# Kernel tuning notes

Hardware: AMD Instinct MI355X
Metric: run time of the kernel (lower is better)

## Reference

```python
import jax, jax.numpy as jnp
import numpy as np

T, B, D, H = 512, 64, 1024, 8
DH = D // H
LN_EPS = 1e-5


def setup_inputs() -> dict:
    ks = jax.random.split(jax.random.key(0), 12)
    s = 1.0 / np.sqrt(D)
    return {
        "x_real": jax.random.normal(ks[0], (T, B, D), jnp.float32),
        "x_imag": jax.random.normal(ks[1], (T, B, D), jnp.float32),
        "value_state": jnp.zeros((B, H, DH), jnp.float32),
        "t": jnp.arange(T, dtype=jnp.int64) if jax.config.jax_enable_x64 else jnp.arange(T, dtype=jnp.int32),
        # ComplexLinear input_proj (bias=True): weight layout [out, in] like torch
        "Wr_in": jax.random.normal(ks[2], (D, D), jnp.float32) * s,
        "Wi_in": jax.random.normal(ks[3], (D, D), jnp.float32) * s,
        "br_in": jax.random.normal(ks[4], (D,), jnp.float32) * 0.01,
        "bi_in": jax.random.normal(ks[5], (D,), jnp.float32) * 0.01,
        # LayerNorm affine
        "ln_gamma": jnp.ones((D,), jnp.float32),
        "ln_beta": jnp.zeros((D,), jnp.float32),
        # QKV linear (bias=False), torch layout [3D, D]
        "W_qkv": jax.random.normal(ks[6], (3 * D, D), jnp.float32) * s,
        # per-head EMA gate logits: log(alpha/(1-alpha)) with alpha=0.9
        "log_alpha": jnp.full((H,), float(np.log(0.9 / 0.1)), jnp.float32),
        # ComplexLinear output_proj (bias=False)
        "Wr_out": jax.random.normal(ks[7], (D, D), jnp.float32) * s,
        "Wi_out": jax.random.normal(ks[8], (D, D), jnp.float32) * s,
    }


def reference(x_real, x_imag, value_state, t, Wr_in, Wi_in, br_in, bi_in,
              ln_gamma, ln_beta, W_qkv, log_alpha, Wr_out, Wi_out):
    scale = jnp.asarray(np.sqrt(DH), x_real.dtype)
    alpha = jax.nn.sigmoid(log_alpha)[None, :, None]  # [1,H,1]

    def step(state, xs):
        xr, xi = xs  # [B,D] each
        # ComplexLinear input projection
        pr = xr @ Wr_in.T - xi @ Wi_in.T + br_in
        pi = xr @ Wi_in.T + xi @ Wr_in.T + bi_in
        xc = pr + pi
        # LayerNorm over last dim
        mu = xc.mean(-1, keepdims=True)
        var = ((xc - mu) ** 2).mean(-1, keepdims=True)
        xc = (xc - mu) * jax.lax.rsqrt(var + LN_EPS) * ln_gamma + ln_beta
        # QKV
        qkv = (xc @ W_qkv.T).reshape(-1, 3, H, DH)
        q, k, v = qkv[:, 0], qkv[:, 1], qkv[:, 2]  # [B,H,DH]
        # per-head sigmoid-gated EMA state update
        new_state = alpha * v + (1.0 - alpha) * state
        gate = jax.nn.sigmoid(jnp.sum(q * k, axis=-1, keepdims=True) / scale)  # [B,H,1]
        retrieved = (gate * new_state).reshape(-1, D)
        # ComplexLinear output projection with zero imaginary input
        return new_state, (retrieved @ Wr_out.T, retrieved @ Wi_out.T)

    final_state, (out_real, out_imag) = jax.lax.scan(step, value_state, (x_real, x_imag))
    return out_real, out_imag, final_state
```

## Files before the change

### kernel.cpp

```cpp
#include <hip/hip_runtime.h>
#include <stdint.h>

#define T_DIM 512
#define B_DIM 64
#define D_DIM 1024
#define H_DIM 8
#define DH_DIM 128
#define MROWS (T_DIM * B_DIM)

typedef unsigned short u16;
typedef __attribute__((ext_vector_type(8))) __bf16 bf16x8;
typedef __attribute__((ext_vector_type(4))) float f32x4;
typedef __attribute__((ext_vector_type(16))) float f32x16;

__device__ __forceinline__ u16 f2bf(float f) {
  union { float f; uint32_t u; } v; v.f = f;
  uint32_t u = v.u;
  u += 0x7fffu + ((u >> 16) & 1u);
  return (u16)(u >> 16);
}
__device__ __forceinline__ float bf2f(u16 h) {
  union { uint32_t u; float f; } v; v.u = ((uint32_t)h) << 16;
  return v.f;
}

__device__ __forceinline__ void gload16(const void* g, void* l) {
  __builtin_amdgcn_global_load_lds(
      (const __attribute__((address_space(1))) uint32_t*)g,
      (__attribute__((address_space(3))) uint32_t*)l, 16, 0, 0);
}

#define SB()  __builtin_amdgcn_sched_barrier(0)
#define BAR() __builtin_amdgcn_s_barrier()
#define VM4() asm volatile("s_waitcnt vmcnt(4)" ::: "memory")
#define VM6() asm volatile("s_waitcnt vmcnt(6)" ::: "memory")
#define PRIO1() __builtin_amdgcn_s_setprio(1)
#define PRIO0() __builtin_amdgcn_s_setprio(0)


__global__ void cast_bf16_kernel(const float* __restrict__ in, u16* __restrict__ out, size_t n8) {
  size_t i = (size_t)blockIdx.x * blockDim.x + threadIdx.x;
  const size_t stride = (size_t)gridDim.x * blockDim.x;
  for (; i < n8; i += stride) {
    const float4 a = ((const float4*)in)[i * 2];
    const float4 b = ((const float4*)in)[i * 2 + 1];
    union { u16 h[8]; uint4 u; } o;
    o.h[0] = f2bf(a.x); o.h[1] = f2bf(a.y); o.h[2] = f2bf(a.z); o.h[3] = f2bf(a.w);
    o.h[4] = f2bf(b.x); o.h[5] = f2bf(b.y); o.h[6] = f2bf(b.z); o.h[7] = f2bf(b.w);
    ((uint4*)out)[i] = o.u;
  }
}

__global__ void prep_wc_kernel(const float* __restrict__ Wr, const float* __restrict__ Wi,
                               u16* __restrict__ Wc) {
  const int idx = blockIdx.x * 256 + threadIdx.x;
  const int n = idx >> 11;
  const int k = idx & 2047;
  const int kk = k & 1023;
  const float a = Wr[n * 1024 + kk], b = Wi[n * 1024 + kk];
  Wc[idx] = f2bf(k < 1024 ? a + b : a - b);
}

__global__ void prep_bc_kernel(const float* __restrict__ br, const float* __restrict__ bi,
                               float* __restrict__ bc) {
  const int i = blockIdx.x * 256 + threadIdx.x;
  if (i < D_DIM) bc[i] = br[i] + bi[i];
}


__device__ __forceinline__ void readF(bf16x8 (&d)[2][2], const u16* s, int rowoff, int la32, int puA) {
#pragma unroll
  for (int mf = 0; mf < 2; ++mf)
#pragma unroll
    for (int kk = 0; kk < 2; ++kk)
      d[mf][kk] = *(const bf16x8*)(s + (rowoff + mf * 32 + la32) * 32 + (puA ^ (kk << 4)));
}

__device__ __forceinline__ void mfma8(f32x16 (&acc)[4][2], const bf16x8 (&a)[2][2],
                                      const bf16x8 (&b)[2][2], int QM) {
#pragma unroll
  for (int kk = 0; kk < 2; ++kk)
#pragma unroll
    for (int mf = 0; mf < 2; ++mf)
#pragma unroll
      for (int nf = 0; nf < 2; ++nf)
        acc[QM * 2 + mf][nf] =
            __builtin_amdgcn_mfma_f32_32x32x16_bf16(a[mf][kk], b[nf][kk], acc[QM * 2 + mf][nf], 0, 0, 0);
}

template <int EPI>
__global__ __launch_bounds__(512, 2) void gemm256_kernel(
    const u16* __restrict__ A0, const u16* __restrict__ A1, int kSplit, int lda,
    const u16* __restrict__ Bw, int ldb,
    const float* __restrict__ bias,
    void* __restrict__ C0, void* __restrict__ C1, void* __restrict__ C2,
    int ldc, int K, int nColBlk)
{
  extern __shared__ u16 lds[];
  const int tid  = threadIdx.x;
  const int lane = tid & 63;
  const int w    = tid >> 6;
  const int wr   = w >> 2;
  const int wc   = w & 3;

  const int bid   = blockIdx.x;
  const int xcd   = bid & 7;
  const int local = bid >> 3;
  const int rowL  = local / nColBlk;
  const int colB  = local - rowL * nColBlk;
  const size_t rowBase = (size_t)(xcd * 16 + rowL) * 256;
  const size_t colBase = (size_t)colB * 256;

  f32x16 acc[4][2];
#pragma unroll
  for (int i = 0; i < 4; ++i)
#pragma unroll
    for (int j = 0; j < 2; ++j)
#pragma unroll
      for (int e = 0; e < 16; ++e) acc[i][j][e] = 0.f;

  const int NT = K >> 6;
  const int la32 = lane & 31;
  const int g2   = lane >> 5;
  const int f    = (la32 & 3) ^ ((la32 >> 2) & 3);
  const int puA  = ((g2 ^ f) << 3);

  auto stageA = [&](int buf, int ks, int t) {
    if (t >= NT) t = 0;
    const int kb = t * 64;
    const u16* Ab; int kc;
    if (kb < kSplit) { Ab = A0; kc = kb; } else { Ab = A1; kc = kb - kSplit; }
    u16* dst = lds + buf * 32768 + ks * 8192;
#pragma unroll
    for (int i2 = 0; i2 < 2; ++i2) {
      const int l = i2 * 512 + tid, r = l >> 2, p = l & 3;
      const int lu = p ^ (r & 3) ^ ((r >> 2) & 3);
      gload16(Ab + (rowBase + r) * (size_t)lda + kc + ks * 32 + lu * 8, dst + l * 8);
    }
  };
  auto stageB = [&](int buf, int ks, int t) {
    if (t >= NT) t = 0;
    const int kb = t * 64;
    u16* dst = lds + buf * 32768 + 16384 + ks * 8192;
#pragma unroll
    for (int i2 = 0; i2 < 2; ++i2) {
      const int l = i2 * 512 + tid, r = l >> 2, p = l & 3;
      const int lu = p ^ (r & 3) ^ ((r >> 2) & 3);
      gload16(Bw + (colBase + r) * (size_t)ldb + kb + ks * 32 + lu * 8, dst + l * 8);
    }
  };

  const u16* sA_b0k0 = lds;
  const u16* sA_b0k1 = lds + 8192;
  const u16* sB_b0k0 = lds + 16384;
  const u16* sB_b0k1 = lds + 16384 + 8192;
  const u16* sA_b1k0 = lds + 32768;
  const u16* sA_b1k1 = lds + 32768 + 8192;
  const u16* sB_b1k0 = lds + 32768 + 16384;
  const u16* sB_b1k1 = lds + 32768 + 16384 + 8192;
  const int rA0 = wr * 128;
  const int rA1 = wr * 128 + 64;
  const int rB  = wc * 64;

  stageA(0, 0, 0); stageB(0, 0, 0); stageA(0, 1, 0); stageB(0, 1, 0);
  stageA(1, 0, 1); stageB(1, 0, 1);
  VM4();
  SB(); BAR(); SB();

  bf16x8 a0[2][2], a1[2][2], bbE[2][2], bbO[2][2];
  const int NIT = NT >> 1;
  for (int i = 0; i < NIT; ++i) {
    const int u = 2 * i, v = 2 * i + 1;
    readF(a0,  sA_b0k0, rA0, la32, puA);
    readF(bbE, sB_b0k0, rB,  la32, puA);
    readF(a1,  sA_b0k0, rA1, la32, puA);
    stageA(1, 1, v);
    SB(); BAR(); SB();
    PRIO1(); mfma8(acc, a0, bbE, 0); PRIO0(); SB();
    BAR(); SB();
    readF(a0,  sA_b0k1, rA0, la32, puA);
    readF(bbO, sB_b0k1, rB,  la32, puA);
    stageB(1, 1, v);
    SB(); BAR(); SB();
    PRIO1(); mfma8(acc, a1, bbE, 1); PRIO0(); SB();
    BAR(); SB();
    readF(a1,  sA_b0k1, rA1, la32, puA);
    stageA(0, 0, u + 2);
    SB(); BAR(); SB();
    PRIO1(); mfma8(acc, a0, bbO, 0); PRIO0(); SB();
    VM6();
    BAR(); SB();
    readF(a0,  sA_b1k0, rA0, la32, puA);
    readF(bbE, sB_b1k0, rB,  la32, puA);
    stageB(0, 0, u + 2);
    SB(); BAR(); SB();
    PRIO1(); mfma8(acc, a1, bbO, 1); PRIO0(); SB();
    VM4();
    BAR(); SB();
    readF(a1,  sA_b1k0, rA1, la32, puA);
    stageA(0, 1, u + 2);
    SB(); BAR(); SB();
    PRIO1(); mfma8(acc, a0, bbE, 0); PRIO0(); SB();
    BAR(); SB();
    readF(a0,  sA_b1k1, rA0, la32, puA);
    readF(bbO, sB_b1k1, rB,  la32, puA);
    stageB(0, 1, u + 2);
    SB(); BAR(); SB();
    PRIO1(); mfma8(acc, a1, bbE, 1); PRIO0(); SB();
    BAR(); SB();
    readF(a1,  sA_b1k1, rA1, la32, puA);
    stageA(1, 0, v + 2);
    SB(); BAR(); SB();
    PRIO1(); mfma8(acc, a0, bbO, 0); PRIO0(); SB();
    BAR(); SB();
    stageB(1, 0, v + 2);
    SB(); BAR(); SB();
    PRIO1(); mfma8(acc, a1, bbO, 1); PRIO0(); SB();
    VM4();
    BAR(); SB();
  }

  const int seg = (int)(colBase >> 10);
  const size_t colSeg = colBase & 1023;
  void* Cout;
  if (EPI == 3)      Cout = (seg == 0) ? C0 : (seg == 1) ? C1 : C2;
  else if (EPI == 2) Cout = (seg == 0) ? C0 : C1;
  else               Cout = C0;

#pragma unroll
  for (int mi = 0; mi < 4; ++mi)
#pragma unroll
    for (int ni = 0; ni < 2; ++ni) {
      const int cn = wc * 64 + ni * 32 + la32;
      const float badd = (EPI == 1) ? bias[colBase + cn] : 0.0f;
      const size_t col = colSeg + cn;
#pragma unroll
      for (int r = 0; r < 16; ++r) {
        const size_t row = rowBase + wr * 128 + mi * 32 + (r & 3) + 8 * (r >> 2) + 4 * g2;
        const float v = acc[mi][ni][r] + badd;
        if (EPI == 2) ((float*)Cout)[row * (size_t)ldc + col] = v;
        else          ((u16*)Cout)[row * (size_t)ldc + col] = f2bf(v);
      }
    }
}


__global__ __launch_bounds__(256) void ln_kernel(u16* __restrict__ xc,
    const float* __restrict__ gamma, const float* __restrict__ beta)
{
  const size_t row = blockIdx.x;
  u16* p = xc + row * D_DIM;
  const int tid = threadIdx.x;
  const int c = tid * 4;
  const uint2 raw = *(const uint2*)(p + c);
  const float v0 = bf2f((u16)(raw.x & 0xffff)), v1 = bf2f((u16)(raw.x >> 16));
  const float v2 = bf2f((u16)(raw.y & 0xffff)), v3 = bf2f((u16)(raw.y >> 16));
  float s = v0 + v1 + v2 + v3;
  float q = v0 * v0 + v1 * v1 + v2 * v2 + v3 * v3;
#pragma unroll
  for (int o = 32; o > 0; o >>= 1) { s += __shfl_xor(s, o); q += __shfl_xor(q, o); }
  __shared__ float red[8];
  if ((tid & 63) == 0) { red[(tid >> 6) * 2] = s; red[(tid >> 6) * 2 + 1] = q; }
  __syncthreads();
  s = red[0] + red[2] + red[4] + red[6];
  q = red[1] + red[3] + red[5] + red[7];
  const float mu = s * (1.0f / D_DIM);
  const float var = q * (1.0f / D_DIM) - mu * mu;
  const float rstd = 1.0f / sqrtf(var + 1e-5f);
  const float y0 = (v0 - mu) * rstd * gamma[c] + beta[c];
  const float y1 = (v1 - mu) * rstd * gamma[c + 1] + beta[c + 1];
  const float y2 = (v2 - mu) * rstd * gamma[c + 2] + beta[c + 2];
  const float y3 = (v3 - mu) * rstd * gamma[c + 3] + beta[c + 3];
  const uint32_t o0 = (uint32_t)f2bf(y0) | ((uint32_t)f2bf(y1) << 16);
  const uint32_t o1 = (uint32_t)f2bf(y2) | ((uint32_t)f2bf(y3) << 16);
  *(uint2*)(p + c) = make_uint2(o0, o1);
}


__global__ __launch_bounds__(256) void gate_kernel(
    const u16* __restrict__ Q, const u16* __restrict__ Kb, float* __restrict__ gate)
{
  const int gw = blockIdx.x * 4 + (threadIdx.x >> 6);
  const int lane = threadIdx.x & 63;
  const size_t row = (size_t)(gw >> 3);
  const int h = gw & 7;
  const size_t off = row * D_DIM + h * DH_DIM + lane * 2;
  const uint32_t qr = *(const uint32_t*)(Q + off);
  const uint32_t kr = *(const uint32_t*)(Kb + off);
  float d = bf2f((u16)(qr & 0xffff)) * bf2f((u16)(kr & 0xffff))
          + bf2f((u16)(qr >> 16))    * bf2f((u16)(kr >> 16));
#pragma unroll
  for (int o = 32; o > 0; o >>= 1) d += __shfl_xor(d, o);
  if (lane == 0) {
    const float x = d * 0.08838834764831845f;
    gate[gw] = 1.0f / (1.0f + expf(-x));
  }
}


__global__ __launch_bounds__(256) void scan_kernel(
    const u16* __restrict__ vb, const float* __restrict__ gate,
    const float* __restrict__ vstate, const float* __restrict__ log_alpha,
    u16* __restrict__ ret, float* __restrict__ fstate)
{
  const int gid = blockIdx.x * 256 + threadIdx.x;
  const int b = gid >> 10;
  const int c = gid & 1023;
  const int h = c >> 7;
  const float alpha = 1.0f / (1.0f + expf(-log_alpha[h]));
  const float oma = 1.0f - alpha;
  float state = vstate[gid];
  const u16* vp = vb + (size_t)b * D_DIM + c;
  u16* rp = ret + (size_t)b * D_DIM + c;
  const float* gp = gate + b * H_DIM + h;
#pragma unroll 4
  for (int t = 0; t < T_DIM; ++t) {
    const float v = bf2f(vp[(size_t)t * (B_DIM * D_DIM)]);
    const float g = gp[(size_t)t * (B_DIM * H_DIM)];
    state = alpha * v + oma * state;
    rp[(size_t)t * (B_DIM * D_DIM)] = f2bf(g * state);
  }
  fstate[gid] = state;
}


extern "C" void kernel_launch(void* const* d_in, const int* in_sizes, int n_in,
                              void* d_out, int out_size, void* d_ws, size_t ws_size,
                              hipStream_t stream) {
  const float* x_real      = (const float*)d_in[0];
  const float* x_imag      = (const float*)d_in[1];
  const float* value_state = (const float*)d_in[2];
  const float* Wr_in  = (const float*)d_in[4];
  const float* Wi_in  = (const float*)d_in[5];
  const float* br_in  = (const float*)d_in[6];
  const float* bi_in  = (const float*)d_in[7];
  const float* ln_g   = (const float*)d_in[8];
  const float* ln_b   = (const float*)d_in[9];
  const float* W_qkv  = (const float*)d_in[10];
  const float* log_alpha = (const float*)d_in[11];
  const float* Wr_out = (const float*)d_in[12];
  const float* Wi_out = (const float*)d_in[13];

  float* out_real = (float*)d_out;
  float* out_imag = out_real + (size_t)MROWS * D_DIM;
  float* fstate   = out_imag + (size_t)MROWS * D_DIM;

  u16* R0a = (u16*)d_out;
  u16* xc  = (u16*)((char*)d_out + (size_t)MROWS * D_DIM * 2);
  u16* Vb  = (u16*)out_imag;

  char* ws = (char*)d_ws;
  size_t off = 0;
  auto alloc = [&](size_t bytes) { void* p = ws + off; off += (bytes + 255) & ~(size_t)255; return p; };
  u16*   Wc    = (u16*)alloc((size_t)1024 * 2048 * 2);
  u16*   Wqkvb = (u16*)alloc((size_t)3072 * 1024 * 2);
  u16*   Wob   = (u16*)alloc((size_t)2048 * 1024 * 2);
  float* bc    = (float*)alloc((size_t)D_DIM * 4);
  u16*   R0b   = (u16*)alloc((size_t)MROWS * D_DIM * 2);
  float* gate  = (float*)alloc((size_t)MROWS * H_DIM * 4);

  const int LDSB = 131072;
  hipFuncSetAttribute((const void*)gemm256_kernel<1>, hipFuncAttributeMaxDynamicSharedMemorySize, LDSB);
  hipFuncSetAttribute((const void*)gemm256_kernel<2>, hipFuncAttributeMaxDynamicSharedMemorySize, LDSB);
  hipFuncSetAttribute((const void*)gemm256_kernel<3>, hipFuncAttributeMaxDynamicSharedMemorySize, LDSB);

  prep_wc_kernel<<<(1024 * 2048) / 256, 256, 0, stream>>>(Wr_in, Wi_in, Wc);
  prep_bc_kernel<<<4, 256, 0, stream>>>(br_in, bi_in, bc);
  cast_bf16_kernel<<<1536, 256, 0, stream>>>(W_qkv, Wqkvb, (size_t)3072 * 1024 / 8);
  cast_bf16_kernel<<<512, 256, 0, stream>>>(Wr_out, Wob, (size_t)1024 * 1024 / 8);
  cast_bf16_kernel<<<512, 256, 0, stream>>>(Wi_out, Wob + (size_t)1024 * 1024, (size_t)1024 * 1024 / 8);
  cast_bf16_kernel<<<4096, 256, 0, stream>>>(x_real, R0a, (size_t)MROWS * D_DIM / 8);
  cast_bf16_kernel<<<4096, 256, 0, stream>>>(x_imag, R0b, (size_t)MROWS * D_DIM / 8);

  gemm256_kernel<1><<<dim3(128 * 4), 512, LDSB, stream>>>(
      R0a, R0b, 1024, 1024, Wc, 2048, bc, xc, nullptr, nullptr, 1024, 2048, 4);
  ln_kernel<<<MROWS, 256, 0, stream>>>(xc, ln_g, ln_b);
  gemm256_kernel<3><<<dim3(128 * 12), 512, LDSB, stream>>>(
      xc, xc, 1024, 1024, Wqkvb, 1024, nullptr, R0a, R0b, Vb, 1024, 1024, 12);
  gate_kernel<<<(MROWS * H_DIM) / 4, 256, 0, stream>>>(R0a, R0b, gate);
  scan_kernel<<<(B_DIM * D_DIM) / 256, 256, 0, stream>>>(Vb, gate, value_state, log_alpha, R0b, fstate);
  gemm256_kernel<2><<<dim3(128 * 8), 512, LDSB, stream>>>(
      R0b, R0b, 1024, 1024, Wob, 1024, nullptr, out_real, out_imag, nullptr, 1024, 1024, 8);
}
```

Measured before the change: 750.8 us.

## Split EMA scan into chunked two-pass scan and merge prep/cast launches

Replaces the sequential 512-step per-channel scan, which ran only 256 blocks, with a two-pass chunked scan. Pass one computes a local carry for each of 8 time chunks, and pass two combines the prior carries using oma^64 before rescanning its chunk, giving 8x more parallelism. The v tensor is read twice and a carry buffer is added. The separate weight-prep and cast kernels are also merged into two launches to cut launch overhead.

```diff
diff --git a/kernel.cpp b/kernel.cpp
--- a/kernel.cpp
+++ b/kernel.cpp
@@ -38,33 +38,49 @@
 #define PRIO0() __builtin_amdgcn_s_setprio(0)
 
 
-__global__ void cast_bf16_kernel(const float* __restrict__ in, u16* __restrict__ out, size_t n8) {
-  size_t i = (size_t)blockIdx.x * blockDim.x + threadIdx.x;
-  const size_t stride = (size_t)gridDim.x * blockDim.x;
-  for (; i < n8; i += stride) {
-    const float4 a = ((const float4*)in)[i * 2];
-    const float4 b = ((const float4*)in)[i * 2 + 1];
-    union { u16 h[8]; uint4 u; } o;
-    o.h[0] = f2bf(a.x); o.h[1] = f2bf(a.y); o.h[2] = f2bf(a.z); o.h[3] = f2bf(a.w);
-    o.h[4] = f2bf(b.x); o.h[5] = f2bf(b.y); o.h[6] = f2bf(b.z); o.h[7] = f2bf(b.w);
-    ((uint4*)out)[i] = o.u;
-  }
-}
-
-__global__ void prep_wc_kernel(const float* __restrict__ Wr, const float* __restrict__ Wi,
-                               u16* __restrict__ Wc) {
-  const int idx = blockIdx.x * 256 + threadIdx.x;
-  const int n = idx >> 11;
-  const int k = idx & 2047;
-  const int kk = k & 1023;
-  const float a = Wr[n * 1024 + kk], b = Wi[n * 1024 + kk];
-  Wc[idx] = f2bf(k < 1024 ? a + b : a - b);
-}
-
-__global__ void prep_bc_kernel(const float* __restrict__ br, const float* __restrict__ bi,
-                               float* __restrict__ bc) {
-  const int i = blockIdx.x * 256 + threadIdx.x;
-  if (i < D_DIM) bc[i] = br[i] + bi[i];
+__device__ __forceinline__ void cast8(const float* __restrict__ in, u16* __restrict__ out, size_t i) {
+  const float4 a = ((const float4*)in)[i * 2];
+  const float4 b = ((const float4*)in)[i * 2 + 1];
+  union { u16 h[8]; uint4 u; } o;
+  o.h[0] = f2bf(a.x); o.h[1] = f2bf(a.y); o.h[2] = f2bf(a.z); o.h[3] = f2bf(a.w);
+  o.h[4] = f2bf(b.x); o.h[5] = f2bf(b.y); o.h[6] = f2bf(b.z); o.h[7] = f2bf(b.w);
+  ((uint4*)out)[i] = o.u;
+}
+
+__global__ void prep_all_kernel(const float* __restrict__ Wr, const float* __restrict__ Wi,
+                                const float* __restrict__ br, const float* __restrict__ bi,
+                                const float* __restrict__ Wqkv,
+                                const float* __restrict__ Wro, const float* __restrict__ Wio,
+                                u16* __restrict__ Wc, float* __restrict__ bc,
+                                u16* __restrict__ Wqkvb, u16* __restrict__ Wob) {
+  const int blk = blockIdx.x;
+  if (blk < 8192) {
+    const int idx = blk * 256 + threadIdx.x;
+    const int n = idx >> 11;
+    const int k = idx & 2047;
+    const int kk = k & 1023;
+    const float a = Wr[n * 1024 + kk], b = Wi[n * 1024 + kk];
+    Wc[idx] = f2bf(k < 1024 ? a + b : a - b);
+  } else if (blk < 9728) {
+    cast8(Wqkv, Wqkvb, (size_t)(blk - 8192) * 256 + threadIdx.x);
+  } else if (blk < 10240) {
+    cast8(Wro, Wob, (size_t)(blk - 9728) * 256 + threadIdx.x);
+  } else if (blk < 10752) {
+    cast8(Wio, Wob + (size_t)1024 * 1024, (size_t)(blk - 10240) * 256 + threadIdx.x);
+  } else {
+    const int i = (blk - 10752) * 256 + threadIdx.x;
+    if (i < D_DIM) bc[i] = br[i] + bi[i];
+  }
+}
+
+__global__ void cast2_kernel(const float* __restrict__ xr, const float* __restrict__ xi,
+                             u16* __restrict__ outr, u16* __restrict__ outi) {
+  int blk = blockIdx.x;
+  const float* src; u16* dst;
+  if (blk < 4096) { src = xr; dst = outr; } else { src = xi; dst = outi; blk -= 4096; }
+  const size_t base = (size_t)blk * 1024 + threadIdx.x;
+#pragma unroll
+  for (int q = 0; q < 4; ++q) cast8(src, dst, base + q * 256);
 }
 
 
@@ -298,29 +314,65 @@
 }
 
 
-__global__ __launch_bounds__(256) void scan_kernel(
-    const u16* __restrict__ vb, const float* __restrict__ gate,
-    const float* __restrict__ vstate, const float* __restrict__ log_alpha,
-    u16* __restrict__ ret, float* __restrict__ fstate)
+__global__ __launch_bounds__(256) void scan1_kernel(
+    const u16* __restrict__ vb, const float* __restrict__ log_alpha,
+    float* __restrict__ carry)
 {
-  const int gid = blockIdx.x * 256 + threadIdx.x;
+  const int j  = blockIdx.x >> 7;
+  const int th = (blockIdx.x & 127) * 256 + threadIdx.x;
+  const int gid = th * 2;
   const int b = gid >> 10;
   const int c = gid & 1023;
   const int h = c >> 7;
   const float alpha = 1.0f / (1.0f + expf(-log_alpha[h]));
   const float oma = 1.0f - alpha;
-  float state = vstate[gid];
-  const u16* vp = vb + (size_t)b * D_DIM + c;
-  u16* rp = ret + (size_t)b * D_DIM + c;
-  const float* gp = gate + b * H_DIM + h;
+  const u16* vp = vb + ((size_t)(4096 * j + b)) * 1024 + c;
+  float s0 = 0.f, s1 = 0.f;
+#pragma unroll 8
+  for (int i = 0; i < 64; ++i) {
+    const uint32_t uv = *(const uint32_t*)(vp + (size_t)i * 65536);
+    s0 = alpha * bf2f((u16)(uv & 0xffff)) + oma * s0;
+    s1 = alpha * bf2f((u16)(uv >> 16))    + oma * s1;
+  }
+  *(float2*)(carry + (size_t)j * 65536 + gid) = make_float2(s0, s1);
+}
+
+__global__ __launch_bounds__(256) void scan2_kernel(
+    const u16* __restrict__ vb, const float* __restrict__ gate,
+    const float* __restrict__ vstate, const float* __restrict__ log_alpha,
+    const float* __restrict__ carry,
+    u16* __restrict__ ret, float* __restrict__ fstate)
+{
+  const int j  = blockIdx.x >> 7;
+  const int th = (blockIdx.x & 127) * 256 + threadIdx.x;
+  const int gid = th * 2;
+  const int b = gid >> 10;
+  const int c = gid & 1023;
+  const int h = c >> 7;
+  const float alpha = 1.0f / (1.0f + expf(-log_alpha[h]));
+  const float oma = 1.0f - alpha;
+  float o64 = oma;
+#pragma unroll
+  for (int q = 0; q < 6; ++q) o64 *= o64;
+  float s0 = vstate[gid], s1 = vstate[gid + 1];
+  for (int i = 0; i < j; ++i) {
+    const float2 L = *(const float2*)(carry + (size_t)i * 65536 + gid);
+    s0 = L.x + o64 * s0;
+    s1 = L.y + o64 * s1;
+  }
+  const u16* vp = vb + ((size_t)(4096 * j + b)) * 1024 + c;
+  u16* rp = ret + ((size_t)(4096 * j + b)) * 1024 + c;
+  const float* gp = gate + (size_t)(4096 * j + b) * H_DIM + h;
 #pragma unroll 4
-  for (int t = 0; t < T_DIM; ++t) {
-    const float v = bf2f(vp[(size_t)t * (B_DIM * D_DIM)]);
-    const float g = gp[(size_t)t * (B_DIM * H_DIM)];
-    state = alpha * v + oma * state;
-    rp[(size_t)t * (B_DIM * D_DIM)] = f2bf(g * state);
-  }
-  fstate[gid] = state;
+  for (int i = 0; i < 64; ++i) {
+    const uint32_t uv = *(const uint32_t*)(vp + (size_t)i * 65536);
+    const float g = gp[(size_t)i * 512];
+    s0 = alpha * bf2f((u16)(uv & 0xffff)) + oma * s0;
+    s1 = alpha * bf2f((u16)(uv >> 16))    + oma * s1;
+    const uint32_t o = (uint32_t)f2bf(g * s0) | ((uint32_t)f2bf(g * s1) << 16);
+    *(uint32_t*)(rp + (size_t)i * 65536) = o;
+  }
+  if (j == 7) { fstate[gid] = s0; fstate[gid + 1] = s1; }
 }
 
 
@@ -358,19 +410,16 @@
   float* bc    = (float*)alloc((size_t)D_DIM * 4);
   u16*   R0b   = (u16*)alloc((size_t)MROWS * D_DIM * 2);
   float* gate  = (float*)alloc((size_t)MROWS * H_DIM * 4);
+  float* carry = (float*)alloc((size_t)8 * B_DIM * D_DIM * 4);
 
   const int LDSB = 131072;
   hipFuncSetAttribute((const void*)gemm256_kernel<1>, hipFuncAttributeMaxDynamicSharedMemorySize, LDSB);
   hipFuncSetAttribute((const void*)gemm256_kernel<2>, hipFuncAttributeMaxDynamicSharedMemorySize, LDSB);
   hipFuncSetAttribute((const void*)gemm256_kernel<3>, hipFuncAttributeMaxDynamicSharedMemorySize, LDSB);
 
-  prep_wc_kernel<<<(1024 * 2048) / 256, 256, 0, stream>>>(Wr_in, Wi_in, Wc);
-  prep_bc_kernel<<<4, 256, 0, stream>>>(br_in, bi_in, bc);
-  cast_bf16_kernel<<<1536, 256, 0, stream>>>(W_qkv, Wqkvb, (size_t)3072 * 1024 / 8);
-  cast_bf16_kernel<<<512, 256, 0, stream>>>(Wr_out, Wob, (size_t)1024 * 1024 / 8);
-  cast_bf16_kernel<<<512, 256, 0, stream>>>(Wi_out, Wob + (size_t)1024 * 1024, (size_t)1024 * 1024 / 8);
-  cast_bf16_kernel<<<4096, 256, 0, stream>>>(x_real, R0a, (size_t)MROWS * D_DIM / 8);
-  cast_bf16_kernel<<<4096, 256, 0, stream>>>(x_imag, R0b, (size_t)MROWS * D_DIM / 8);
+  prep_all_kernel<<<10756, 256, 0, stream>>>(Wr_in, Wi_in, br_in, bi_in, W_qkv, Wr_out, Wi_out,
+                                             Wc, bc, Wqkvb, Wob);
+  cast2_kernel<<<8192, 256, 0, stream>>>(x_real, x_imag, R0a, R0b);
 
   gemm256_kernel<1><<<dim3(128 * 4), 512, LDSB, stream>>>(
       R0a, R0b, 1024, 1024, Wc, 2048, bc, xc, nullptr, nullptr, 1024, 2048, 4);
@@ -378,7 +427,8 @@
   gemm256_kernel<3><<<dim3(128 * 12), 512, LDSB, stream>>>(
       xc, xc, 1024, 1024, Wqkvb, 1024, nullptr, R0a, R0b, Vb, 1024, 1024, 12);
   gate_kernel<<<(MROWS * H_DIM) / 4, 256, 0, stream>>>(R0a, R0b, gate);
-  scan_kernel<<<(B_DIM * D_DIM) / 256, 256, 0, stream>>>(Vb, gate, value_state, log_alpha, R0b, fstate);
+  scan1_kernel<<<1024, 256, 0, stream>>>(Vb, log_alpha, carry);
+  scan2_kernel<<<1024, 256, 0, stream>>>(Vb, gate, value_state, log_alpha, carry, R0b, fstate);
   gemm256_kernel<2><<<dim3(128 * 8), 512, LDSB, stream>>>(
       R0b, R0b, 1024, 1024, Wob, 1024, nullptr, out_real, out_imag, nullptr, 1024, 1024, 8);
 }
```

Result: faster. 706.3 us (-5.9%).
